# Optimization experiments

Measured on AMD Instinct MI355X. Metric: run time of the kernel, lower is better.

## Reference

```python
import jax, jax.numpy as jnp
import numpy as np

B, T, D_IN, D_H, R = 64, 512, 1024, 1024, 16
IN_DIMS = (8, 8, 16)    # 8*8*16 = 1024 = input_size (and hidden_size)
OUT_DIMS = (16, 16, 16)  # 16*16*16 = 4096 = 4*hidden_size


def setup_inputs() -> dict:
    key = jax.random.key(0)
    ks = jax.random.split(key, 14)
    s = 0.5 / np.sqrt(R)  # keep TT product well-scaled

    def cores(k):
        k1, k2, k3, k4, k5, k6 = jax.random.split(k, 6)
        i1, i2, i3 = IN_DIMS
        o1, o2, o3 = OUT_DIMS
        return (
            jax.random.normal(k1, (i1, R)) * s,        # rank-1 boundary squeezed
            jax.random.normal(k2, (R, i2, R)) * s,
            jax.random.normal(k3, (R, i3, R)) * s,
            jax.random.normal(k4, (R, o1, R)) * s,
            jax.random.normal(k5, (R, o2, R)) * s,
            jax.random.normal(k6, (R, o3)) * s,        # rank-1 boundary squeezed
        )

    ih = cores(ks[0])
    hh = cores(ks[1])
    return {
        "x": jax.random.normal(ks[2], (B, T, D_IN), dtype=jnp.float32),
        "ih_g1": ih[0], "ih_g2": ih[1], "ih_g3": ih[2],
        "ih_g4": ih[3], "ih_g5": ih[4], "ih_g6": ih[5],
        "hh_g1": hh[0], "hh_g2": hh[1], "hh_g3": hh[2],
        "hh_g4": hh[3], "hh_g5": hh[4], "hh_g6": hh[5],
        "b_ih": jnp.zeros((4 * D_H,), jnp.float32),
        "b_hh": jnp.zeros((4 * D_H,), jnp.float32),
    }


def tt_matvec(x, g1, g2, g3, g4, g5, g6):
    # x: (B, in_features) -> (B, out_features) via TT weight contraction
    b = x.shape[0]
    t = x.reshape(b, *IN_DIMS)                      # (B, i1, i2, i3)
    t = jnp.einsum('bijk,ia->bjka', t, g1)          # contract in-mode 1
    t = jnp.einsum('bjka,ajc->bkc', t, g2)          # contract in-mode 2
    t = jnp.einsum('bkc,ckd->bd', t, g3)            # contract in-mode 3
    t = jnp.einsum('bd,dne->bne', t, g4)            # expand out-mode 1
    t = jnp.einsum('bne,emf->bnmf', t, g5)          # expand out-mode 2
    t = jnp.einsum('bnmf,fp->bnmp', t, g6)          # expand out-mode 3
    return t.reshape(b, -1)


def reference(x, ih_g1, ih_g2, ih_g3, ih_g4, ih_g5, ih_g6,
              hh_g1, hh_g2, hh_g3, hh_g4, hh_g5, hh_g6, b_ih, b_hh):
    ih_cores = (ih_g1, ih_g2, ih_g3, ih_g4, ih_g5, ih_g6)
    hh_cores = (hh_g1, hh_g2, hh_g3, hh_g4, hh_g5, hh_g6)
    batch = x.shape[0]
    h0 = jnp.zeros((batch, D_H), x.dtype)
    c0 = jnp.zeros((batch, D_H), x.dtype)

    # precompute input-to-hidden projections for all timesteps (batched)
    ih_all = tt_matvec(x.reshape(-1, D_IN), *ih_cores).reshape(batch, -1, 4 * D_H) + b_ih
    ih_all = jnp.swapaxes(ih_all, 0, 1)  # (T, B, 4H)

    def step(carry, ih_t):
        h, c = carry
        gates = ih_t + tt_matvec(h, *hh_cores) + b_hh
        i, f, g, o = jnp.split(gates, 4, axis=1)
        c = jax.nn.sigmoid(f) * c + jax.nn.sigmoid(i) * jnp.tanh(g)
        h = jax.nn.sigmoid(o) * jnp.tanh(c)
        return (h, c), h

    (h, c), hs = jax.lax.scan(step, (h0, c0), ih_all)
    output = jnp.swapaxes(hs, 0, 1)  # (B, T, H)
    return output, (h, c)
```

## Files before the change

### kernel.cpp

```cpp
#include <hip/hip_runtime.h>
#include <math.h>

#define NB   64
#define NT   512
#define DH   1024
#define HID_OFF  33554432
#define HC_SZ    65536


typedef float v2f __attribute__((ext_vector_type(2)));

__device__ __forceinline__ v2f mkv2(float a, float b) { v2f r; r.x = a; r.y = b; return r; }

__device__ __forceinline__ void bar_lgkm() {
    asm volatile("s_waitcnt lgkmcnt(0)\n\ts_barrier" ::: "memory");
}

template<int CTRL>
__device__ __forceinline__ float dpp_add(float v) {
    int m = __builtin_amdgcn_update_dpp(0, __builtin_bit_cast(int, v), CTRL, 0xf, 0xf, true);
    return v + __builtin_bit_cast(float, m);
}
__device__ __forceinline__ float wave_red_sum(float v) {
    v = dpp_add<0x111>(v);
    v = dpp_add<0x112>(v);
    v = dpp_add<0x114>(v);
    v = dpp_add<0x118>(v);
    v = dpp_add<0x142>(v);
    v = dpp_add<0x143>(v);
    return v;
}

__device__ __forceinline__ float sigm(float x) { return 1.f / (1.f + __expf(-x)); }
__device__ __forceinline__ float tanh_fast(float x) {
    float e = __expf(2.f * x);
    return 1.f - 2.f / (e + 1.f);
}

__global__ __launch_bounds__(256) void k0_build(
    const float* __restrict__ g1a, const float* __restrict__ g2a,
    const float* __restrict__ g3a, const float* __restrict__ g5a,
    const float* __restrict__ g6a,
    const float* __restrict__ g1b, const float* __restrict__ g2b,
    const float* __restrict__ g3b, const float* __restrict__ g5b,
    const float* __restrict__ g6b,
    float* __restrict__ ATa, float* __restrict__ M2a,
    float* __restrict__ ATb, float* __restrict__ M2b)
{
    const float* g1 = blockIdx.x ? g1b : g1a;
    const float* g2 = blockIdx.x ? g2b : g2a;
    const float* g3 = blockIdx.x ? g3b : g3a;
    const float* g5 = blockIdx.x ? g5b : g5a;
    const float* g6 = blockIdx.x ? g6b : g6a;
    float* A_T = blockIdx.x ? ATb : ATa;
    float* M2  = blockIdx.x ? M2b : M2a;

    __shared__ float Lg1[128], Lg2[2048], Lg3[4096], Lg5[4096], Lg6[256], M1[1024];
    int tid = threadIdx.x;
    for (int i = tid; i < 128;  i += 256) Lg1[i] = g1[i];
    for (int i = tid; i < 2048; i += 256) Lg2[i] = g2[i];
    for (int i = tid; i < 4096; i += 256) Lg3[i] = g3[i];
    for (int i = tid; i < 4096; i += 256) Lg5[i] = g5[i];
    for (int i = tid; i < 256;  i += 256) Lg6[i] = g6[i];
    __syncthreads();
    for (int idx = tid; idx < 1024; idx += 256) {
        int i1 = idx >> 7, j = (idx >> 4) & 7, c = idx & 15;
        float s = 0.f;
        for (int a = 0; a < 16; ++a) s += Lg1[i1 * 16 + a] * Lg2[a * 128 + j * 16 + c];
        M1[idx] = s;
    }
    __syncthreads();
    int base = 4096 * blockIdx.y;
    for (int idx = base + tid; idx < base + 4096; idx += 256) {
        int d = idx >> 10, i = idx & 1023;
        int i1 = i >> 7, j = (i >> 4) & 7, k = i & 15;
        float s = 0.f;
        for (int c = 0; c < 16; ++c) s += M1[i1 * 128 + j * 16 + c] * Lg3[c * 256 + k * 16 + d];
        A_T[idx] = s;
    }
    if (blockIdx.y == 0) {
        for (int idx = tid; idx < 4096; idx += 256) {
            int e = idx >> 8, mp = idx & 255;
            int m = mp >> 4, p = mp & 15;
            float s = 0.f;
            for (int f = 0; f < 16; ++f) s += Lg5[e * 256 + m * 16 + f] * Lg6[f * 16 + p];
            M2[idx] = s;
        }
    }
}

__global__ __launch_bounds__(256) void k0b_whh(
    const float* __restrict__ g4hh, const float* __restrict__ M2hh,
    float* __restrict__ Whh2)
{
    int n = blockIdx.x;
    int mp = threadIdx.x;
    __shared__ float Ls[256];
    Ls[mp] = g4hh[(mp >> 4) * 256 + n * 16 + (mp & 15)];
    float m2loc[16];
    #pragma unroll
    for (int e = 0; e < 16; ++e) m2loc[e] = M2hh[e * 256 + mp];
    __syncthreads();
    float wv[16];
    #pragma unroll
    for (int d = 0; d < 16; ++d) {
        float s = 0.f;
        #pragma unroll
        for (int e = 0; e < 16; ++e) s = fmaf(Ls[d * 16 + e], m2loc[e], s);
        wv[d] = s;
    }
    float4* dst = (float4*)&Whh2[(size_t)(n * 256 + mp) * 16];
    dst[0] = make_float4(wv[0], wv[1], wv[2], wv[3]);
    dst[1] = make_float4(wv[4], wv[5], wv[6], wv[7]);
    dst[2] = make_float4(wv[8], wv[9], wv[10], wv[11]);
    dst[3] = make_float4(wv[12], wv[13], wv[14], wv[15]);
}

__global__ __launch_bounds__(256) void k1_zy(
    const float* __restrict__ x, const float* __restrict__ A_T,
    const float* __restrict__ g4, float* __restrict__ y_out)
{
    __shared__ __align__(16) float Z[2][2][2][16];

    const int tid  = threadIdx.x;
    const int lane = tid & 63;
    const int w    = tid >> 6;
    const int s    = w >> 1;
    const int wp   = w & 1;
    const int i0   = wp * 512 + lane * 8;

    v2f av[8][8];
    #pragma unroll
    for (int d = 0; d < 16; ++d) {
        float Ar[8];
        *(float4*)&Ar[0] = *(const float4*)&A_T[d * 1024 + i0];
        *(float4*)&Ar[4] = *(const float4*)&A_T[d * 1024 + i0 + 4];
        #pragma unroll
        for (int ip = 0; ip < 8; ++ip) {
            if (d & 1) av[ip][d >> 1].y = Ar[ip];
            else       av[ip][d >> 1].x = Ar[ip];
        }
    }
    const int u0 = wp * 128 + lane;
    const int u1 = u0 + 64;
    float g4r0[16], g4r1[16];
    #pragma unroll
    for (int d = 0; d < 16; ++d) {
        g4r0[d] = g4[d * 256 + u0];
        g4r1[d] = g4[d * 256 + u1];
    }

    const int rbase = (blockIdx.x * 2 + s) * 16;
    float xr[8];
    *(float4*)&xr[0] = *(const float4*)&x[(size_t)rbase * 1024 + i0];
    *(float4*)&xr[4] = *(const float4*)&x[(size_t)rbase * 1024 + i0 + 4];

    for (int rr = 0; rr < 16; ++rr) {
        const int row = rbase + rr;
        const int rp  = rr & 1;
        float xn[8];
        if (rr < 15) {
            *(float4*)&xn[0] = *(const float4*)&x[(size_t)(row + 1) * 1024 + i0];
            *(float4*)&xn[4] = *(const float4*)&x[(size_t)(row + 1) * 1024 + i0 + 4];
        }
        v2f p[8];
        #pragma unroll
        for (int dd = 0; dd < 8; ++dd) p[dd] = xr[0] * av[0][dd];
        #pragma unroll
        for (int ip = 1; ip < 8; ++ip)
            #pragma unroll
            for (int dd = 0; dd < 8; ++dd) p[dd] += xr[ip] * av[ip][dd];
        #pragma unroll
        for (int dd = 0; dd < 8; ++dd) {
            float sx = wave_red_sum(p[dd].x);
            float sy = wave_red_sum(p[dd].y);
            if (lane == 63) *(v2f*)&Z[s][rp][wp][2 * dd] = mkv2(sx, sy);
        }
        bar_lgkm();
        float zs[16];
        {
            const float4* za = (const float4*)&Z[s][rp][0][0];
            const float4* zb = (const float4*)&Z[s][rp][1][0];
            float4 a0 = za[0], a1 = za[1], a2 = za[2], a3 = za[3];
            float4 b0 = zb[0], b1 = zb[1], b2 = zb[2], b3 = zb[3];
            *(float4*)&zs[0]  = make_float4(a0.x + b0.x, a0.y + b0.y, a0.z + b0.z, a0.w + b0.w);
            *(float4*)&zs[4]  = make_float4(a1.x + b1.x, a1.y + b1.y, a1.z + b1.z, a1.w + b1.w);
            *(float4*)&zs[8]  = make_float4(a2.x + b2.x, a2.y + b2.y, a2.z + b2.z, a2.w + b2.w);
            *(float4*)&zs[12] = make_float4(a3.x + b3.x, a3.y + b3.y, a3.z + b3.z, a3.w + b3.w);
        }
        float y0 = zs[0] * g4r0[0], y1 = zs[0] * g4r1[0];
        #pragma unroll
        for (int d = 1; d < 16; ++d) {
            y0 = fmaf(zs[d], g4r0[d], y0);
            y1 = fmaf(zs[d], g4r1[d], y1);
        }
        y_out[(size_t)row * 256 + u0] = y0;
        y_out[(size_t)row * 256 + u1] = y1;
        #pragma unroll
        for (int ip = 0; ip < 8; ++ip) xr[ip] = xn[ip];
    }
}

__global__ __launch_bounds__(1024, 4) void k2_lstm(
    const float* __restrict__ A_T_hh, const float* __restrict__ Whh2,
    const float* __restrict__ M2ih, const float* __restrict__ y_ih_g,
    const float* __restrict__ b_ih, const float* __restrict__ b_hh,
    float* __restrict__ pfdump, float* __restrict__ out)
{
    __shared__ __align__(16) float Lh[1024];
    __shared__ __align__(16) float Lzp[2][2][16];

    const int tid  = threadIdx.x;
    const int b    = blockIdx.x;
    const int lane = tid & 63;
    const int w    = tid >> 6;
    const int dg   = w >> 1;
    const int wsl  = w & 1;
    const int mp   = tid & 255;
    const int n0   = tid >> 8;

    const int ibase = wsl * 512 + 2 * lane;
    v2f a0p[4], a1p[4];
    #pragma unroll
    for (int k = 0; k < 4; ++k) {
        a0p[k] = *(const v2f*)&A_T_hh[(2 * dg) * 1024 + ibase + 128 * k];
        a1p[k] = *(const v2f*)&A_T_hh[(2 * dg + 1) * 1024 + ibase + 128 * k];
    }

    v2f whh[4][8];
    #pragma unroll
    for (int g = 0; g < 4; ++g) {
        const float4* wr4 = (const float4*)&Whh2[(size_t)((n0 + 4 * g) * 256 + mp) * 16];
        float4 f0 = wr4[0], f1 = wr4[1], f2 = wr4[2], f3 = wr4[3];
        whh[g][0] = mkv2(f0.x, f0.y); whh[g][1] = mkv2(f0.z, f0.w);
        whh[g][2] = mkv2(f1.x, f1.y); whh[g][3] = mkv2(f1.z, f1.w);
        whh[g][4] = mkv2(f2.x, f2.y); whh[g][5] = mkv2(f2.z, f2.w);
        whh[g][6] = mkv2(f3.x, f3.y); whh[g][7] = mkv2(f3.z, f3.w);
    }
    float m2i[16];
    #pragma unroll
    for (int e = 0; e < 16; ++e) m2i[e] = M2ih[e * 256 + mp];
    float bias0 = b_ih[tid]        + b_hh[tid];
    float bias1 = b_ih[1024 + tid] + b_hh[1024 + tid];
    float bias2 = b_ih[2048 + tid] + b_hh[2048 + tid];
    float bias3 = b_ih[3072 + tid] + b_hh[3072 + tid];

    Lh[tid] = 0.f;
    float h = 0.f, c = 0.f;
    __syncthreads();

    const float* yrow = y_ih_g + (size_t)b * (NT * 256);
    float*       orow = out + (size_t)b * (NT * 1024);
    float pfacc = 0.f;

    for (int t = 0; t < NT; ++t) {
        const int p = t & 1;

        const int ybase = __builtin_amdgcn_readfirstlane(t * 256 + n0 * 16);
        float yv[4][16];
        #pragma unroll
        for (int g = 0; g < 4; ++g)
            #pragma unroll
            for (int e = 0; e < 16; ++e)
                yv[g][e] = yrow[ybase + g * 64 + e];
        float ypf = 0.f;
        {
            int tpf = (t + 4 < NT) ? (t + 4) : (NT - 1);
            if (tid < 256) ypf = yrow[tpf * 256 + tid];
        }

        float p0, p1;
        {
            const v2f* hv2 = (const v2f*)&Lh[ibase];
            v2f hp0 = hv2[0], hp1 = hv2[64], hp2 = hv2[128], hp3 = hv2[192];
            v2f s0 = hp0 * a0p[0]; s0 += hp1 * a0p[1]; s0 += hp2 * a0p[2]; s0 += hp3 * a0p[3];
            v2f s1 = hp0 * a1p[0]; s1 += hp1 * a1p[1]; s1 += hp2 * a1p[2]; s1 += hp3 * a1p[3];
            p0 = s0.x + s0.y;
            p1 = s1.x + s1.y;
        }
        p0 = wave_red_sum(p0);
        p1 = wave_red_sum(p1);
        if (lane == 63) *(v2f*)&Lzp[p][wsl][2 * dg] = mkv2(p0, p1);

        float acc0 = bias0, acc1 = bias1, acc2 = bias2, acc3 = bias3;
        #pragma unroll
        for (int e = 0; e < 16; ++e) {
            acc0 = fmaf(yv[0][e], m2i[e], acc0);
            acc1 = fmaf(yv[1][e], m2i[e], acc1);
            acc2 = fmaf(yv[2][e], m2i[e], acc2);
            acc3 = fmaf(yv[3][e], m2i[e], acc3);
        }
        bar_lgkm();

        float zs[16];
        {
            const float4* za = (const float4*)&Lzp[p][0][0];
            const float4* zb = (const float4*)&Lzp[p][1][0];
            float4 a0 = za[0], a1 = za[1], a2 = za[2], a3 = za[3];
            float4 b0 = zb[0], b1 = zb[1], b2 = zb[2], b3 = zb[3];
            *(float4*)&zs[0]  = make_float4(a0.x + b0.x, a0.y + b0.y, a0.z + b0.z, a0.w + b0.w);
            *(float4*)&zs[4]  = make_float4(a1.x + b1.x, a1.y + b1.y, a1.z + b1.z, a1.w + b1.w);
            *(float4*)&zs[8]  = make_float4(a2.x + b2.x, a2.y + b2.y, a2.z + b2.z, a2.w + b2.w);
            *(float4*)&zs[12] = make_float4(a3.x + b3.x, a3.y + b3.y, a3.z + b3.z, a3.w + b3.w);
        }
        {
            const v2f* zp = (const v2f*)zs;
            v2f A0 = zp[0] * whh[0][0], A1 = zp[0] * whh[1][0];
            v2f A2 = zp[0] * whh[2][0], A3 = zp[0] * whh[3][0];
            #pragma unroll
            for (int k = 1; k < 8; ++k) {
                A0 += zp[k] * whh[0][k];
                A1 += zp[k] * whh[1][k];
                A2 += zp[k] * whh[2][k];
                A3 += zp[k] * whh[3][k];
            }
            acc0 += A0.x + A0.y;
            acc1 += A1.x + A1.y;
            acc2 += A2.x + A2.y;
            acc3 += A3.x + A3.y;
        }

        float ig = sigm(acc0);
        float fg = sigm(acc1);
        float gg = tanh_fast(acc2);
        float og = sigm(acc3);
        c = fg * c + ig * gg;
        h = og * tanh_fast(c);

        Lh[tid] = h;
        orow[t * 1024 + tid] = h;
        pfacc += ypf;
        bar_lgkm();
    }

    out[HID_OFF + b * 1024 + tid] = h;
    out[HID_OFF + HC_SZ + b * 1024 + tid] = c;
    if (tid < 256) pfdump[tid] = pfacc;
}

extern "C" void kernel_launch(void* const* d_in, const int* in_sizes, int n_in,
                              void* d_out, int out_size, void* d_ws, size_t ws_size,
                              hipStream_t stream) {
    const float* x     = (const float*)d_in[0];
    const float* ihg1  = (const float*)d_in[1];
    const float* ihg2  = (const float*)d_in[2];
    const float* ihg3  = (const float*)d_in[3];
    const float* ihg4  = (const float*)d_in[4];
    const float* ihg5  = (const float*)d_in[5];
    const float* ihg6  = (const float*)d_in[6];
    const float* hhg1  = (const float*)d_in[7];
    const float* hhg2  = (const float*)d_in[8];
    const float* hhg3  = (const float*)d_in[9];
    const float* hhg4  = (const float*)d_in[10];
    const float* hhg5  = (const float*)d_in[11];
    const float* hhg6  = (const float*)d_in[12];
    const float* b_ih  = (const float*)d_in[13];
    const float* b_hh  = (const float*)d_in[14];
    float* out = (float*)d_out;

    float* ws     = (float*)d_ws;
    float* ATih   = ws;
    float* AThh   = ws + 16384;
    float* M2ih   = ws + 32768;
    float* M2hh   = ws + 36864;
    float* Whh2   = ws + 40960;
    float* pfdump = ws + 106496;
    float* yih    = ws + 107520;

    hipLaunchKernelGGL(k0_build, dim3(2, 4), dim3(256), 0, stream,
                       ihg1, ihg2, ihg3, ihg5, ihg6,
                       hhg1, hhg2, hhg3, hhg5, hhg6,
                       ATih, M2ih, AThh, M2hh);
    hipLaunchKernelGGL(k0b_whh, dim3(16), dim3(256), 0, stream,
                       hhg4, M2hh, Whh2);
    hipLaunchKernelGGL(k1_zy, dim3(1024), dim3(256), 0, stream,
                       x, ATih, ihg4, yih);
    hipLaunchKernelGGL(k2_lstm, dim3(NB), dim3(1024), 0, stream,
                       AThh, Whh2, M2ih, yih, b_ih, b_hh, pfdump, out);
}
```

Before: 1.652 ms.

## Unfuse hidden-to-hidden g4·M2 product into two-stage contraction via LDS in LSTM loop

Drops the precomputed Whh2 matrix (g4 folded into M2) and its build kernel. Each recurrent step now first contracts z with g4 per wave and writes the 256 results to shared memory, then every thread contracts those with its M2 column. This cuts per-thread register weights from 64 to 32 floats, easing register pressure, and removes one launch. The cost is an extra barrier and LDS round-trip on the serial per-timestep critical path.

```diff
diff --git a/kernel.cpp b/kernel.cpp
--- a/kernel.cpp
+++ b/kernel.cpp
@@ -89,33 +89,6 @@
     }
 }
 
-__global__ __launch_bounds__(256) void k0b_whh(
-    const float* __restrict__ g4hh, const float* __restrict__ M2hh,
-    float* __restrict__ Whh2)
-{
-    int n = blockIdx.x;
-    int mp = threadIdx.x;
-    __shared__ float Ls[256];
-    Ls[mp] = g4hh[(mp >> 4) * 256 + n * 16 + (mp & 15)];
-    float m2loc[16];
-    #pragma unroll
-    for (int e = 0; e < 16; ++e) m2loc[e] = M2hh[e * 256 + mp];
-    __syncthreads();
-    float wv[16];
-    #pragma unroll
-    for (int d = 0; d < 16; ++d) {
-        float s = 0.f;
-        #pragma unroll
-        for (int e = 0; e < 16; ++e) s = fmaf(Ls[d * 16 + e], m2loc[e], s);
-        wv[d] = s;
-    }
-    float4* dst = (float4*)&Whh2[(size_t)(n * 256 + mp) * 16];
-    dst[0] = make_float4(wv[0], wv[1], wv[2], wv[3]);
-    dst[1] = make_float4(wv[4], wv[5], wv[6], wv[7]);
-    dst[2] = make_float4(wv[8], wv[9], wv[10], wv[11]);
-    dst[3] = make_float4(wv[12], wv[13], wv[14], wv[15]);
-}
-
 __global__ __launch_bounds__(256) void k1_zy(
     const float* __restrict__ x, const float* __restrict__ A_T,
     const float* __restrict__ g4, float* __restrict__ y_out)
@@ -201,14 +174,18 @@
     }
 }
 
-__global__ __launch_bounds__(1024, 4) void k2_lstm(
-    const float* __restrict__ A_T_hh, const float* __restrict__ Whh2,
+__global__ __launch_bounds__(1024)
+__attribute__((amdgpu_waves_per_eu(4, 4)))
+void k2_lstm(
+    const float* __restrict__ A_T_hh, const float* __restrict__ g4hh,
+    const float* __restrict__ M2hh,
     const float* __restrict__ M2ih, const float* __restrict__ y_ih_g,
     const float* __restrict__ b_ih, const float* __restrict__ b_hh,
     float* __restrict__ pfdump, float* __restrict__ out)
 {
     __shared__ __align__(16) float Lh[1024];
     __shared__ __align__(16) float Lzp[2][2][16];
+    __shared__ __align__(16) float Lw[2][256];
 
     const int tid  = threadIdx.x;
     const int b    = blockIdx.x;
@@ -227,19 +204,19 @@
         a1p[k] = *(const v2f*)&A_T_hh[(2 * dg + 1) * 1024 + ibase + 128 * k];
     }
 
-    v2f whh[4][8];
-    #pragma unroll
-    for (int g = 0; g < 4; ++g) {
-        const float4* wr4 = (const float4*)&Whh2[(size_t)((n0 + 4 * g) * 256 + mp) * 16];
-        float4 f0 = wr4[0], f1 = wr4[1], f2 = wr4[2], f3 = wr4[3];
-        whh[g][0] = mkv2(f0.x, f0.y); whh[g][1] = mkv2(f0.z, f0.w);
-        whh[g][2] = mkv2(f1.x, f1.y); whh[g][3] = mkv2(f1.z, f1.w);
-        whh[g][4] = mkv2(f2.x, f2.y); whh[g][5] = mkv2(f2.z, f2.w);
-        whh[g][6] = mkv2(f3.x, f3.y); whh[g][7] = mkv2(f3.z, f3.w);
-    }
+    float g4w[16];
+    #pragma unroll
+    for (int d = 0; d < 16; ++d) g4w[d] = g4hh[d * 256 + w * 16 + (lane & 15)];
+
+    v2f m2v[8];
+    #pragma unroll
+    for (int k = 0; k < 8; ++k)
+        m2v[k] = mkv2(M2hh[(2 * k) * 256 + mp], M2hh[(2 * k + 1) * 256 + mp]);
+
     float m2i[16];
     #pragma unroll
     for (int e = 0; e < 16; ++e) m2i[e] = M2ih[e * 256 + mp];
+
     float bias0 = b_ih[tid]        + b_hh[tid];
     float bias1 = b_ih[1024 + tid] + b_hh[1024 + tid];
     float bias2 = b_ih[2048 + tid] + b_hh[2048 + tid];
@@ -292,8 +269,8 @@
         }
         bar_lgkm();
 
-        float zs[16];
         {
+            float zs[16];
             const float4* za = (const float4*)&Lzp[p][0][0];
             const float4* zb = (const float4*)&Lzp[p][1][0];
             float4 a0 = za[0], a1 = za[1], a2 = za[2], a3 = za[3];
@@ -302,22 +279,33 @@
             *(float4*)&zs[4]  = make_float4(a1.x + b1.x, a1.y + b1.y, a1.z + b1.z, a1.w + b1.w);
             *(float4*)&zs[8]  = make_float4(a2.x + b2.x, a2.y + b2.y, a2.z + b2.z, a2.w + b2.w);
             *(float4*)&zs[12] = make_float4(a3.x + b3.x, a3.y + b3.y, a3.z + b3.z, a3.w + b3.w);
-        }
-        {
-            const v2f* zp = (const v2f*)zs;
-            v2f A0 = zp[0] * whh[0][0], A1 = zp[0] * whh[1][0];
-            v2f A2 = zp[0] * whh[2][0], A3 = zp[0] * whh[3][0];
+            float wa = zs[0] * g4w[0], wb = zs[1] * g4w[1];
             #pragma unroll
-            for (int k = 1; k < 8; ++k) {
-                A0 += zp[k] * whh[0][k];
-                A1 += zp[k] * whh[1][k];
-                A2 += zp[k] * whh[2][k];
-                A3 += zp[k] * whh[3][k];
+            for (int d = 2; d < 16; d += 2) {
+                wa = fmaf(zs[d],     g4w[d],     wa);
+                wb = fmaf(zs[d + 1], g4w[d + 1], wb);
             }
-            acc0 += A0.x + A0.y;
-            acc1 += A1.x + A1.y;
-            acc2 += A2.x + A2.y;
-            acc3 += A3.x + A3.y;
+            if (lane < 16) Lw[p][w * 16 + lane] = wa + wb;
+        }
+        bar_lgkm();
+
+        #pragma unroll
+        for (int g = 0; g < 4; ++g) {
+            const float4* wr4 = (const float4*)&Lw[p][(n0 + 4 * g) * 16];
+            float4 f0 = wr4[0], f1 = wr4[1], f2 = wr4[2], f3 = wr4[3];
+            v2f A = mkv2(f0.x, f0.y) * m2v[0];
+            A += mkv2(f0.z, f0.w) * m2v[1];
+            A += mkv2(f1.x, f1.y) * m2v[2];
+            A += mkv2(f1.z, f1.w) * m2v[3];
+            A += mkv2(f2.x, f2.y) * m2v[4];
+            A += mkv2(f2.z, f2.w) * m2v[5];
+            A += mkv2(f3.x, f3.y) * m2v[6];
+            A += mkv2(f3.z, f3.w) * m2v[7];
+            float d1 = A.x + A.y;
+            if (g == 0) acc0 += d1;
+            else if (g == 1) acc1 += d1;
+            else if (g == 2) acc2 += d1;
+            else acc3 += d1;
         }
 
         float ig = sigm(acc0);
@@ -363,7 +351,6 @@
     float* AThh   = ws + 16384;
     float* M2ih   = ws + 32768;
     float* M2hh   = ws + 36864;
-    float* Whh2   = ws + 40960;
     float* pfdump = ws + 106496;
     float* yih    = ws + 107520;
 
@@ -371,10 +358,8 @@
                        ihg1, ihg2, ihg3, ihg5, ihg6,
                        hhg1, hhg2, hhg3, hhg5, hhg6,
                        ATih, M2ih, AThh, M2hh);
-    hipLaunchKernelGGL(k0b_whh, dim3(16), dim3(256), 0, stream,
-                       hhg4, M2hh, Whh2);
     hipLaunchKernelGGL(k1_zy, dim3(1024), dim3(256), 0, stream,
                        x, ATih, ihg4, yih);
     hipLaunchKernelGGL(k2_lstm, dim3(NB), dim3(1024), 0, stream,
-                       AThh, Whh2, M2ih, yih, b_ih, b_hh, pfdump, out);
-}
+                       AThh, hhg4, M2hh, M2ih, yih, b_ih, b_hh, pfdump, out);
+}
```

Measured after the change: 1.421 ms. 14.0% less time.
